# Kernel tuning notes

Measured on AMD Instinct MI355X. Metric: run time of the kernel, lower is better.

## Reference

```python
import jax, jax.numpy as jnp
import numpy as np

EPS = 1e-12  # F.normalize eps
WIN_SIZE = 200
WIN_STEP = 30  # eval mode (training uses 10)
N_WIN = 30     # 31 windows from length-1100 axis, last one dropped


def setup_inputs() -> dict:
    key = jax.random.key(0)
    ks = jax.random.split(key, 6)
    dim, K, out_dim = 128, 64, 256
    N, H, W = 8, 16, 900
    s = 1.0 / np.sqrt(dim)
    return {
        "x": jax.random.normal(ks[0], (N, dim, H, W), dtype=jnp.float32),
        "cluster_centers": jax.random.uniform(ks[1], (K, dim), dtype=jnp.float32),
        "conv_w": jax.random.normal(ks[2], (K, dim), dtype=jnp.float32) * s,
        "conv_b": jax.random.normal(ks[3], (K,), dtype=jnp.float32) * s,
        "mlp_w": jax.random.normal(ks[4], (out_dim, K * dim), dtype=jnp.float32) * s,
        "mlp_b": jax.random.normal(ks[5], (out_dim,), dtype=jnp.float32) * s,
    }


def _l2norm(v, axis):
    return v / jnp.clip(jnp.linalg.norm(v, axis=axis, keepdims=True), EPS)


def reference(x, cluster_centers, conv_w, conv_b, mlp_w, mlp_b):
    N, C, H, W = x.shape
    K = conv_w.shape[0]
    # 1x1 conv -> soft assignment, softmax over clusters (dim=1 after view(N,K,HW))
    logits = jnp.einsum('nchw,kc->nkhw', x, conv_w) + conv_b[None, :, None, None]
    a = jax.nn.softmax(logits, axis=1)  # (N,K,H,W)
    # Fused weighted residual sum over H (torch sums dim=-2 of (N,K,C,H,W)):
    # vlad_pre[n,k,c,w] = sum_h a[n,k,h,w]*x[n,c,h,w] - centers[k,c]*sum_h a[n,k,h,w]
    wx = jnp.einsum('nkhw,nchw->nkcw', a, x)               # (N,K,C,W)
    asum = a.sum(axis=2)                                    # (N,K,W)
    res = wx - cluster_centers[None, :, :, None] * asum[:, :, None, :]
    # circular pad along yaw: [800:] ++ all ++ [:100] -> length 1100
    res = jnp.concatenate([res[..., 800:], res, res[..., :100]], axis=-1)
    # sliding-window sum, size 200 step 30, drop last window -> 30 windows
    cs = jnp.cumsum(res, axis=-1)
    cs = jnp.concatenate([jnp.zeros(res.shape[:-1] + (1,), res.dtype), cs], axis=-1)
    starts = jnp.arange(N_WIN) * WIN_STEP
    win = cs[..., starts + WIN_SIZE] - cs[..., starts]      # (N,K,C,30)
    vlad = jnp.transpose(win, (0, 3, 1, 2)).reshape(N * N_WIN, K, C)
    vlad = _l2norm(vlad, axis=2)                            # intra-norm per cluster
    vlad = _l2norm(vlad.reshape(N * N_WIN, K * C), axis=1)  # global norm
    out = vlad @ mlp_w.T + mlp_b
    out = _l2norm(out, axis=1)
    return out.reshape(N, N_WIN, -1)
```

## Files before the change

kernel.cpp:

```cpp
#include <hip/hip_runtime.h>
#include <cstddef>

#define EPSF 1e-12f
#define NCB 90
#define NT 30
#define ODIM 256
#define DDIM 8192

typedef unsigned short u16;
typedef __attribute__((ext_vector_type(8))) short short8;
typedef __attribute__((ext_vector_type(4))) float float4v;

__device__ inline u16 f2bf(float f) {
  union { float f; unsigned u; } v; v.f = f;
  unsigned r = v.u + 0x7FFFu + ((v.u >> 16) & 1u);
  return (u16)(r >> 16);
}
__device__ inline float bf2f(u16 h) {
  union { unsigned u; float f; } v; v.u = ((unsigned)h) << 16;
  return v.f;
}

__global__ __launch_bounds__(512, 2) void k1_assign(
    const float* __restrict__ x,
    const float* __restrict__ conv_w,
    const float* __restrict__ conv_b,
    float* __restrict__ P,
    float* __restrict__ PA)
{
  __shared__ __align__(16) char smem[81408];

  const int bx0 = blockIdx.x;
  const int n = bx0 & 7;
  const int q = bx0 >> 3;
  const int t = threadIdx.x;
  const int lane = t & 63;
  const int w8 = t >> 6;

  const float* xn0 = x + (size_t)n * 1843200 + (size_t)(3 * q) * 10;

  const int colt = w8 & 1;
  const int kt = w8 >> 1;
  const int kr = kt * 16 + (lane & 15);
  const float bk = conv_b[kr];

  short8 wh[4], wl[4];
  {
    const int cbase = (lane >> 4) << 3;
#pragma unroll
    for (int cb32 = 0; cb32 < 4; ++cb32) {
      const float* wp = conv_w + (size_t)kr * 128 + cb32 * 32 + cbase;
      float4 u0 = *(const float4*)wp;
      float4 u1 = *(const float4*)(wp + 4);
      float fv[8] = {u0.x, u0.y, u0.z, u0.w, u1.x, u1.y, u1.z, u1.w};
      union { u16 u[8]; short8 v; } hh, ll;
#pragma unroll
      for (int j = 0; j < 8; ++j) {
        u16 h = f2bf(fv[j]);
        hh.u[j] = h;
        ll.u[j] = f2bf(fv[j] - bf2f(h));
      }
      wh[cb32] = hh.v; wl[cb32] = ll.v;
    }
  }

  float4v pacc[3][4];
#pragma unroll
  for (int si = 0; si < 3; ++si)
#pragma unroll
    for (int i = 0; i < 4; ++i) pacc[si][i] = (float4v){0.f, 0.f, 0.f, 0.f};
  float pak[3] = {0.f, 0.f, 0.f};

  float2 xr[3][4];
#pragma unroll
  for (int s = 0; s < 4; ++s) {
    int e2 = t + 512 * s;
    int c = e2 >> 4, p = e2 & 15;
    int cl = 2 * p;
    int h = cl / 10, wi = cl - 10 * h;
    const float* ap = xn0 + (size_t)c * 14400 + h * 900 + wi;
#pragma unroll
    for (int si = 0; si < 3; ++si)
      xr[si][s] = *(const float2*)(ap + si * 10);
  }

  for (int cc = 0; cc < 5; ++cc) {
    __syncthreads();
#pragma unroll
    for (int s = 0; s < 4; ++s) {
      int e2 = t + 512 * s;
      int c = e2 >> 4, p = e2 & 15;
      int cl = 2 * p;
      int ip = (c >> 4) * 640 + (p >> 2) * 160 + (c & 15) * 8 + (cl & 7);
      int F = (p >> 3) * 4 + (c >> 5);
      int L = (((c >> 3) & 3) << 4) + (cl & 15);
      int i0 = F * 520 + L * 8 + (c & 7);
#pragma unroll
      for (int si = 0; si < 3; ++si) {
        u16 h0 = f2bf(xr[si][s].x), h1 = f2bf(xr[si][s].y);
        u16* xf = (u16*)(smem + si * 27136 + 8320);
        u16* xtf = (u16*)(smem + si * 27136);
        ushort2 pr; pr.x = h0; pr.y = h1;
        *(ushort2*)&xf[ip] = pr;
        xtf[i0] = h0;
        xtf[i0 + 8] = h1;
      }
    }
    if (cc < 4) {
#pragma unroll
      for (int s = 0; s < 4; ++s) {
        int e2 = t + 512 * s;
        int c = e2 >> 4, p = e2 & 15;
        int g = (cc + 1) * 32 + 2 * p;
        int h = g / 10, wi = g - 10 * h;
        const float* ap = xn0 + (size_t)c * 14400 + h * 900 + wi;
#pragma unroll
        for (int si = 0; si < 3; ++si)
          xr[si][s] = *(const float2*)(ap + si * 10);
      }
    }
    __syncthreads();

    {
      float4v d0[3];
#pragma unroll
      for (int si = 0; si < 3; ++si) d0[si] = (float4v){0.f, 0.f, 0.f, 0.f};
#pragma unroll
      for (int cb32 = 0; cb32 < 4; ++cb32) {
#pragma unroll
        for (int si = 0; si < 3; ++si) {
          const u16* xtf = (const u16*)(smem + si * 27136);
          short8 xa = *(short8*)&xtf[(colt * 4 + cb32) * 520 + lane * 8];
          d0[si] = __builtin_amdgcn_mfma_f32_16x16x32_bf16(xa, wh[cb32], d0[si], 0, 0, 0);
          d0[si] = __builtin_amdgcn_mfma_f32_16x16x32_bf16(xa, wl[cb32], d0[si], 0, 0, 0);
        }
      }
      int colb = colt * 16 + ((lane >> 4) << 2);
#pragma unroll
      for (int si = 0; si < 3; ++si) {
        float* As = (float*)(smem + si * 27136 + 18560);
#pragma unroll
        for (int r = 0; r < 4; ++r)
          As[kr * 33 + colb + r] = d0[si][r] + bk;
      }
    }
    __syncthreads();

#pragma unroll
    for (int si = 0; si < 3; ++si) {
      float* As = (float*)(smem + si * 27136 + 18560);
      float* invs = (float*)(smem + si * 27136 + 27008);
      u16* afr = (u16*)(smem + si * 27136);
      {
        const int col4 = lane & 3;
        const int kq = lane >> 2;
        const int colg = w8 * 4 + col4;
        float m = -3.4e38f;
#pragma unroll
        for (int i = 0; i < 4; ++i) m = fmaxf(m, As[(kq * 4 + i) * 33 + colg]);
        m = fmaxf(m, __shfl_xor(m, 4));
        m = fmaxf(m, __shfl_xor(m, 8));
        m = fmaxf(m, __shfl_xor(m, 16));
        m = fmaxf(m, __shfl_xor(m, 32));
        float s = 0.f;
#pragma unroll
        for (int i = 0; i < 4; ++i) {
          int a = (kq * 4 + i) * 33 + colg;
          float e = __expf(As[a] - m);
          As[a] = e;
          s += e;
        }
        s += __shfl_xor(s, 4);
        s += __shfl_xor(s, 8);
        s += __shfl_xor(s, 16);
        s += __shfl_xor(s, 32);
        if (kq == 0) invs[colg] = 1.f / s;
      }
      {
        union { u16 u[4]; ushort4 v; } cvt;
        float paks = 0.f;
#pragma unroll
        for (int j = 0; j < 4; ++j) {
          float a = As[lane * 33 + w8 * 4 + j] * invs[w8 * 4 + j];
          paks += a;
          cvt.u[j] = f2bf(a);
        }
        pak[si] += paks;
        int dst = ((lane >> 4) * 64 + ((w8 >> 1) << 4) + (lane & 15)) * 8 + (w8 & 1) * 4;
        *(ushort4*)&afr[dst] = cvt.v;
      }
    }
    __syncthreads();

#pragma unroll
    for (int si = 0; si < 3; ++si) {
      const u16* afr = (const u16*)(smem + si * 27136);
      const u16* xf = (const u16*)(smem + si * 27136 + 8320);
      short8 aa = *(short8*)&afr[((w8 >> 1) * 64 + lane) * 8];
#pragma unroll
      for (int c4 = 0; c4 < 4; ++c4) {
        int ct = (w8 & 1) * 4 + c4;
        short8 xb = *(short8*)&xf[ct * 640 + (lane >> 4) * 160 + (lane & 15) * 8];
        pacc[si][c4] = __builtin_amdgcn_mfma_f32_16x16x32_bf16(aa, xb, pacc[si][c4], 0, 0, 0);
      }
    }
  }

  {
    int krow = (w8 >> 1) * 16 + ((lane >> 4) << 2);
    int c0 = (w8 & 1) * 64 + (lane & 15);
#pragma unroll
    for (int si = 0; si < 3; ++si) {
      float* Pp = P + (size_t)(n * NCB + 3 * q + si) * DDIM;
#pragma unroll
      for (int c4 = 0; c4 < 4; ++c4)
#pragma unroll
        for (int r = 0; r < 4; ++r)
          Pp[(krow + r) * 128 + c0 + c4 * 16] = pacc[si][c4][r];
    }
  }
  __syncthreads();
#pragma unroll
  for (int si = 0; si < 3; ++si)
    ((float*)(smem + si * 27136 + 18560))[t] = pak[si];
  __syncthreads();
  if (t < 64) {
#pragma unroll
    for (int si = 0; si < 3; ++si) {
      const float* pasum = (const float*)(smem + si * 27136 + 18560);
      float s = 0.f;
#pragma unroll
      for (int i = 0; i < 8; ++i) s += pasum[t + 64 * i];
      PA[(size_t)(n * NCB + 3 * q + si) * 64 + t] = s;
    }
  }
}

__global__ __launch_bounds__(256) void k2_vlad(
    const float* __restrict__ P, const float* __restrict__ PA,
    const float* __restrict__ centers, u16* __restrict__ vlad16,
    float* __restrict__ gss)
{
  __shared__ float Ak[8];
  __shared__ float red[4];
  const int bx0 = blockIdx.x;
  const int id = (bx0 & 7) * 240 + (bx0 >> 3);
  const int n = id / 240;
  const int rem = id - n * 240;
  const int wt = rem >> 3, eb = rem & 7;
  const int win = n * NT + wt;
  const int t = threadIdx.x;

  if (t < 32) {
    int kk = t >> 2, ii = t & 3;
    float s = 0.f;
#pragma unroll
    for (int ss = 0; ss < 5; ++ss) {
      int i = ii + 4 * ss;
      int cb = (3 * wt + 80 + i) % 90;
      s += PA[((size_t)n * NCB + cb) * 64 + eb * 8 + kk];
    }
    s += __shfl_xor(s, 1);
    s += __shfl_xor(s, 2);
    if (ii == 0) Ak[kk] = s;
  }
  __syncthreads();

  const int e0 = eb * 1024 + t * 4;
  const float* base = P + (size_t)n * NCB * DDIM + e0;
  float v[4];
#pragma unroll
  for (int j = 0; j < 4; ++j) v[j] = 0.f;
#pragma unroll 5
  for (int i = 0; i < 20; ++i) {
    int cb = (3 * wt + 80 + i) % 90;
    float4 u0 = *(const float4*)(base + (size_t)cb * DDIM);
    v[0] += u0.x; v[1] += u0.y; v[2] += u0.z; v[3] += u0.w;
  }

  const float A = Ak[t >> 5];
  const float* ce = centers + e0;
  float ss8 = 0.f;
#pragma unroll
  for (int j = 0; j < 4; ++j) {
    float val = v[j] - ce[j] * A;
    v[j] = val;
    ss8 += val * val;
  }
  float ssg = ss8;
  ssg += __shfl_xor(ssg, 1);
  ssg += __shfl_xor(ssg, 2);
  ssg += __shfl_xor(ssg, 4);
  ssg += __shfl_xor(ssg, 8);
  ssg += __shfl_xor(ssg, 16);
  float rn = 1.f / fmaxf(sqrtf(ssg), EPSF);
  float ts = ss8 * rn * rn;
  ts += __shfl_xor(ts, 1);
  ts += __shfl_xor(ts, 2);
  ts += __shfl_xor(ts, 4);
  ts += __shfl_xor(ts, 8);
  ts += __shfl_xor(ts, 16);
  ts += __shfl_xor(ts, 32);
  if ((t & 63) == 0) red[t >> 6] = ts;
  __syncthreads();
  if (t == 0) gss[(size_t)win * 8 + eb] = red[0] + red[1] + red[2] + red[3];

  union { u16 u[4]; ushort4 v4; } o;
#pragma unroll
  for (int j = 0; j < 4; ++j) o.u[j] = f2bf(v[j] * rn);
  *(ushort4*)(vlad16 + (size_t)win * DDIM + e0) = o.v4;
}

__global__ __launch_bounds__(256) void k3_gemm(
    const u16* __restrict__ vlad16, const float* __restrict__ gss,
    const float* __restrict__ mlp_w, float* __restrict__ part)
{
  __shared__ float ga[48];
  const int bx = blockIdx.x;
  const int xcd = bx & 7;
  const int q = bx >> 3;
  const int rtg = q % 5;
  const int h = (q / 5) * 8 + xcd;
  const int ot = h & 1;
  const int ks = h >> 1;
  const int t = threadIdx.x;
  const int lane = t & 63;
  const int w = t >> 6;

  if (t < 48) {
    int r = rtg * 48 + t;
    float s = 0.f;
#pragma unroll
    for (int j = 0; j < 8; ++j) s += gss[(size_t)r * 8 + j];
    ga[t] = 1.f / fmaxf(sqrtf(s), EPSF);
  }
  __syncthreads();

  const int m = lane & 15;
  const int kg = lane >> 4;
  const int d0 = ks * 256 + kg * 8;
  const u16* a0 = vlad16 + (size_t)(rtg * 48 + m) * DDIM + d0;

  float4v acc[3][2];
#pragma unroll
  for (int mi = 0; mi < 3; ++mi)
#pragma unroll
    for (int i = 0; i < 2; ++i) acc[mi][i] = (float4v){0.f, 0.f, 0.f, 0.f};

#pragma unroll
  for (int ko = 0; ko < 8; ++ko) {
    short8 a[3];
#pragma unroll
    for (int mi = 0; mi < 3; ++mi)
      a[mi] = *(const short8*)(a0 + (size_t)(mi * 16) * DDIM + ko * 32);
#pragma unroll
    for (int nt = 0; nt < 2; ++nt) {
      int o = ot * 128 + w * 32 + nt * 16 + m;
      const float* wrow = mlp_w + (size_t)o * DDIM + d0 + ko * 32;
      float4 u0 = *(const float4*)wrow;
      float4 u1 = *(const float4*)(wrow + 4);
      union { u16 u[8]; short8 v; } bb;
      bb.u[0] = f2bf(u0.x); bb.u[1] = f2bf(u0.y); bb.u[2] = f2bf(u0.z); bb.u[3] = f2bf(u0.w);
      bb.u[4] = f2bf(u1.x); bb.u[5] = f2bf(u1.y); bb.u[6] = f2bf(u1.z); bb.u[7] = f2bf(u1.w);
#pragma unroll
      for (int mi = 0; mi < 3; ++mi)
        acc[mi][nt] = __builtin_amdgcn_mfma_f32_16x16x32_bf16(a[mi], bb.v, acc[mi][nt], 0, 0, 0);
    }
  }

  float* pp = part + ((size_t)ks * 240 + rtg * 48) * ODIM;
#pragma unroll
  for (int mi = 0; mi < 3; ++mi)
#pragma unroll
    for (int nt = 0; nt < 2; ++nt) {
      int o = ot * 128 + w * 32 + nt * 16 + m;
#pragma unroll
      for (int r = 0; r < 4; ++r) {
        int rl = mi * 16 + kg * 4 + r;
        pp[rl * ODIM + o] = acc[mi][nt][r] * ga[rl];
      }
    }
}

__global__ __launch_bounds__(1024) void k4_out(
    const float* __restrict__ part, const float* __restrict__ bias,
    float* __restrict__ out)
{
  __shared__ float acc[4][256];
  __shared__ float red[4];
  const int r = blockIdx.x;
  const int t = threadIdx.x;
  const int o = t & 255, sq = t >> 8;

  float v = 0.f;
#pragma unroll
  for (int s = 0; s < 8; ++s)
    v += part[((size_t)(sq * 8 + s) * 240 + r) * ODIM + o];
  acc[sq][o] = v;
  __syncthreads();

  float ss = 0.f;
  if (t < 256) {
    v = acc[0][o] + acc[1][o] + acc[2][o] + acc[3][o] + bias[o];
    ss = v * v;
    ss += __shfl_xor(ss, 32);
    ss += __shfl_xor(ss, 16);
    ss += __shfl_xor(ss, 8);
    ss += __shfl_xor(ss, 4);
    ss += __shfl_xor(ss, 2);
    ss += __shfl_xor(ss, 1);
    if ((o & 63) == 0) red[t >> 6] = ss;
  }
  __syncthreads();
  if (t < 256) {
    float total = red[0] + red[1] + red[2] + red[3];
    out[(size_t)r * ODIM + o] = v / fmaxf(sqrtf(total), EPSF);
  }
}

extern "C" void kernel_launch(void* const* d_in, const int* in_sizes, int n_in,
                              void* d_out, int out_size, void* d_ws, size_t ws_size,
                              hipStream_t stream) {
  const float* x       = (const float*)d_in[0];
  const float* centers = (const float*)d_in[1];
  const float* conv_w  = (const float*)d_in[2];
  const float* conv_b  = (const float*)d_in[3];
  const float* mlp_w   = (const float*)d_in[4];
  const float* mlp_b   = (const float*)d_in[5];
  float* out = (float*)d_out;

  float* ws     = (float*)d_ws;
  float* P      = ws;
  float* PA     = ws + 5898240;
  u16*   vlad16 = (u16*)(ws + 5944320);
  float* gss    = (float*)(ws + 6927360);
  float* part   = ws;

  k1_assign<<<dim3(240),        dim3(512),  0, stream>>>(x, conv_w, conv_b, P, PA);
  k2_vlad  <<<dim3(8 * NT * 8), dim3(256),  0, stream>>>(P, PA, centers, vlad16, gss);
  k3_gemm  <<<dim3(320),        dim3(256),  0, stream>>>(vlad16, gss, mlp_w, part);
  k4_out   <<<dim3(240),        dim3(1024), 0, stream>>>(part, mlp_b, out);
}
```

Measured before the change: 154.7 us.

## Fuse four kernels into one cooperative kernel with grid-wide syncs

Merges the assignment, VLAD window/normalization, GEMM and output-normalization kernels into a single cooperative launch of 240 blocks of 512 threads, separated by grid.sync barriers. The later stages are remapped onto the 240 blocks (two 256-thread groups per block for VLAD and GEMM, 160 active blocks for GEMM). This removes three kernel-launch gaps and their tail effects. In exchange it adds grid-barrier cost and reduced parallelism in the later stages, and it relies on all 240 blocks being co-resident.

```diff
diff --git a/kernel.cpp b/kernel.cpp
--- a/kernel.cpp
+++ b/kernel.cpp
@@ -1,5 +1,8 @@
 #include <hip/hip_runtime.h>
+#include <hip/hip_cooperative_groups.h>
 #include <cstddef>
+
+namespace cg = cooperative_groups;
 
 #define EPSF 1e-12f
 #define NCB 90
@@ -21,400 +24,405 @@
   return v.f;
 }
 
-__global__ __launch_bounds__(512, 2) void k1_assign(
+__global__ __launch_bounds__(512, 2) void fused_all(
     const float* __restrict__ x,
     const float* __restrict__ conv_w,
     const float* __restrict__ conv_b,
+    const float* __restrict__ centers,
+    const float* __restrict__ mlp_w,
+    const float* __restrict__ mlp_b,
     float* __restrict__ P,
-    float* __restrict__ PA)
+    float* __restrict__ PA,
+    u16* __restrict__ vlad16,
+    float* __restrict__ gss,
+    float* __restrict__ part,
+    float* __restrict__ out)
 {
+  cg::grid_group grid = cg::this_grid();
   __shared__ __align__(16) char smem[81408];
-
   const int bx0 = blockIdx.x;
-  const int n = bx0 & 7;
-  const int q = bx0 >> 3;
   const int t = threadIdx.x;
   const int lane = t & 63;
   const int w8 = t >> 6;
 
-  const float* xn0 = x + (size_t)n * 1843200 + (size_t)(3 * q) * 10;
-
-  const int colt = w8 & 1;
-  const int kt = w8 >> 1;
-  const int kr = kt * 16 + (lane & 15);
-  const float bk = conv_b[kr];
-
-  short8 wh[4], wl[4];
   {
-    const int cbase = (lane >> 4) << 3;
-#pragma unroll
-    for (int cb32 = 0; cb32 < 4; ++cb32) {
-      const float* wp = conv_w + (size_t)kr * 128 + cb32 * 32 + cbase;
-      float4 u0 = *(const float4*)wp;
-      float4 u1 = *(const float4*)(wp + 4);
-      float fv[8] = {u0.x, u0.y, u0.z, u0.w, u1.x, u1.y, u1.z, u1.w};
-      union { u16 u[8]; short8 v; } hh, ll;
-#pragma unroll
-      for (int j = 0; j < 8; ++j) {
-        u16 h = f2bf(fv[j]);
-        hh.u[j] = h;
-        ll.u[j] = f2bf(fv[j] - bf2f(h));
-      }
-      wh[cb32] = hh.v; wl[cb32] = ll.v;
-    }
-  }
-
-  float4v pacc[3][4];
-#pragma unroll
-  for (int si = 0; si < 3; ++si)
-#pragma unroll
-    for (int i = 0; i < 4; ++i) pacc[si][i] = (float4v){0.f, 0.f, 0.f, 0.f};
-  float pak[3] = {0.f, 0.f, 0.f};
-
-  float2 xr[3][4];
-#pragma unroll
-  for (int s = 0; s < 4; ++s) {
-    int e2 = t + 512 * s;
-    int c = e2 >> 4, p = e2 & 15;
-    int cl = 2 * p;
-    int h = cl / 10, wi = cl - 10 * h;
-    const float* ap = xn0 + (size_t)c * 14400 + h * 900 + wi;
+    const int n = bx0 & 7;
+    const int q = bx0 >> 3;
+
+    const float* xn0 = x + (size_t)n * 1843200 + (size_t)(3 * q) * 10;
+
+    const int colt = w8 & 1;
+    const int kt = w8 >> 1;
+    const int kr = kt * 16 + (lane & 15);
+    const float bk = conv_b[kr];
+
+    short8 wh[4], wl[4];
+    {
+      const int cbase = (lane >> 4) << 3;
+#pragma unroll
+      for (int cb32 = 0; cb32 < 4; ++cb32) {
+        const float* wp = conv_w + (size_t)kr * 128 + cb32 * 32 + cbase;
+        float4 u0 = *(const float4*)wp;
+        float4 u1 = *(const float4*)(wp + 4);
+        float fv[8] = {u0.x, u0.y, u0.z, u0.w, u1.x, u1.y, u1.z, u1.w};
+        union { u16 u[8]; short8 v; } hh, ll;
+#pragma unroll
+        for (int j = 0; j < 8; ++j) {
+          u16 h = f2bf(fv[j]);
+          hh.u[j] = h;
+          ll.u[j] = f2bf(fv[j] - bf2f(h));
+        }
+        wh[cb32] = hh.v; wl[cb32] = ll.v;
+      }
+    }
+
+    float4v pacc[3][4];
 #pragma unroll
     for (int si = 0; si < 3; ++si)
-      xr[si][s] = *(const float2*)(ap + si * 10);
-  }
-
-  for (int cc = 0; cc < 5; ++cc) {
-    __syncthreads();
+#pragma unroll
+      for (int i = 0; i < 4; ++i) pacc[si][i] = (float4v){0.f, 0.f, 0.f, 0.f};
+    float pak[3] = {0.f, 0.f, 0.f};
+
+    float2 xr[3][4];
 #pragma unroll
     for (int s = 0; s < 4; ++s) {
       int e2 = t + 512 * s;
       int c = e2 >> 4, p = e2 & 15;
       int cl = 2 * p;
-      int ip = (c >> 4) * 640 + (p >> 2) * 160 + (c & 15) * 8 + (cl & 7);
-      int F = (p >> 3) * 4 + (c >> 5);
-      int L = (((c >> 3) & 3) << 4) + (cl & 15);
-      int i0 = F * 520 + L * 8 + (c & 7);
-#pragma unroll
-      for (int si = 0; si < 3; ++si) {
-        u16 h0 = f2bf(xr[si][s].x), h1 = f2bf(xr[si][s].y);
-        u16* xf = (u16*)(smem + si * 27136 + 8320);
-        u16* xtf = (u16*)(smem + si * 27136);
-        ushort2 pr; pr.x = h0; pr.y = h1;
-        *(ushort2*)&xf[ip] = pr;
-        xtf[i0] = h0;
-        xtf[i0 + 8] = h1;
-      }
-    }
-    if (cc < 4) {
+      int h = cl / 10, wi = cl - 10 * h;
+      const float* ap = xn0 + (size_t)c * 14400 + h * 900 + wi;
+#pragma unroll
+      for (int si = 0; si < 3; ++si)
+        xr[si][s] = *(const float2*)(ap + si * 10);
+    }
+
+    for (int cc = 0; cc < 5; ++cc) {
+      __syncthreads();
 #pragma unroll
       for (int s = 0; s < 4; ++s) {
         int e2 = t + 512 * s;
         int c = e2 >> 4, p = e2 & 15;
-        int g = (cc + 1) * 32 + 2 * p;
-        int h = g / 10, wi = g - 10 * h;
-        const float* ap = xn0 + (size_t)c * 14400 + h * 900 + wi;
-#pragma unroll
-        for (int si = 0; si < 3; ++si)
-          xr[si][s] = *(const float2*)(ap + si * 10);
-      }
-    }
-    __syncthreads();
-
-    {
-      float4v d0[3];
-#pragma unroll
-      for (int si = 0; si < 3; ++si) d0[si] = (float4v){0.f, 0.f, 0.f, 0.f};
-#pragma unroll
-      for (int cb32 = 0; cb32 < 4; ++cb32) {
+        int cl = 2 * p;
+        int ip = (c >> 4) * 640 + (p >> 2) * 160 + (c & 15) * 8 + (cl & 7);
+        int F = (p >> 3) * 4 + (c >> 5);
+        int L = (((c >> 3) & 3) << 4) + (cl & 15);
+        int i0 = F * 520 + L * 8 + (c & 7);
 #pragma unroll
         for (int si = 0; si < 3; ++si) {
-          const u16* xtf = (const u16*)(smem + si * 27136);
-          short8 xa = *(short8*)&xtf[(colt * 4 + cb32) * 520 + lane * 8];
-          d0[si] = __builtin_amdgcn_mfma_f32_16x16x32_bf16(xa, wh[cb32], d0[si], 0, 0, 0);
-          d0[si] = __builtin_amdgcn_mfma_f32_16x16x32_bf16(xa, wl[cb32], d0[si], 0, 0, 0);
-        }
-      }
-      int colb = colt * 16 + ((lane >> 4) << 2);
+          u16 h0 = f2bf(xr[si][s].x), h1 = f2bf(xr[si][s].y);
+          u16* xf = (u16*)(smem + si * 27136 + 8320);
+          u16* xtf = (u16*)(smem + si * 27136);
+          ushort2 pr; pr.x = h0; pr.y = h1;
+          *(ushort2*)&xf[ip] = pr;
+          xtf[i0] = h0;
+          xtf[i0 + 8] = h1;
+        }
+      }
+      if (cc < 4) {
+#pragma unroll
+        for (int s = 0; s < 4; ++s) {
+          int e2 = t + 512 * s;
+          int c = e2 >> 4, p = e2 & 15;
+          int g = (cc + 1) * 32 + 2 * p;
+          int h = g / 10, wi = g - 10 * h;
+          const float* ap = xn0 + (size_t)c * 14400 + h * 900 + wi;
+#pragma unroll
+          for (int si = 0; si < 3; ++si)
+            xr[si][s] = *(const float2*)(ap + si * 10);
+        }
+      }
+      __syncthreads();
+
+      {
+        float4v d0[3];
+#pragma unroll
+        for (int si = 0; si < 3; ++si) d0[si] = (float4v){0.f, 0.f, 0.f, 0.f};
+#pragma unroll
+        for (int cb32 = 0; cb32 < 4; ++cb32) {
+#pragma unroll
+          for (int si = 0; si < 3; ++si) {
+            const u16* xtf = (const u16*)(smem + si * 27136);
+            short8 xa = *(short8*)&xtf[(colt * 4 + cb32) * 520 + lane * 8];
+            d0[si] = __builtin_amdgcn_mfma_f32_16x16x32_bf16(xa, wh[cb32], d0[si], 0, 0, 0);
+            d0[si] = __builtin_amdgcn_mfma_f32_16x16x32_bf16(xa, wl[cb32], d0[si], 0, 0, 0);
+          }
+        }
+        int colb = colt * 16 + ((lane >> 4) << 2);
+#pragma unroll
+        for (int si = 0; si < 3; ++si) {
+          float* As = (float*)(smem + si * 27136 + 18560);
+#pragma unroll
+          for (int r = 0; r < 4; ++r)
+            As[kr * 33 + colb + r] = d0[si][r] + bk;
+        }
+      }
+      __syncthreads();
+
 #pragma unroll
       for (int si = 0; si < 3; ++si) {
         float* As = (float*)(smem + si * 27136 + 18560);
-#pragma unroll
-        for (int r = 0; r < 4; ++r)
-          As[kr * 33 + colb + r] = d0[si][r] + bk;
+        float* invs = (float*)(smem + si * 27136 + 27008);
+        u16* afr = (u16*)(smem + si * 27136);
+        {
+          const int col4 = lane & 3;
+          const int kq = lane >> 2;
+          const int colg = w8 * 4 + col4;
+          float m = -3.4e38f;
+#pragma unroll
+          for (int i = 0; i < 4; ++i) m = fmaxf(m, As[(kq * 4 + i) * 33 + colg]);
+          m = fmaxf(m, __shfl_xor(m, 4));
+          m = fmaxf(m, __shfl_xor(m, 8));
+          m = fmaxf(m, __shfl_xor(m, 16));
+          m = fmaxf(m, __shfl_xor(m, 32));
+          float s = 0.f;
+#pragma unroll
+          for (int i = 0; i < 4; ++i) {
+            int a = (kq * 4 + i) * 33 + colg;
+            float e = __expf(As[a] - m);
+            As[a] = e;
+            s += e;
+          }
+          s += __shfl_xor(s, 4);
+          s += __shfl_xor(s, 8);
+          s += __shfl_xor(s, 16);
+          s += __shfl_xor(s, 32);
+          if (kq == 0) invs[colg] = 1.f / s;
+        }
+        {
+          union { u16 u[4]; ushort4 v; } cvt;
+          float paks = 0.f;
+#pragma unroll
+          for (int j = 0; j < 4; ++j) {
+            float a = As[lane * 33 + w8 * 4 + j] * invs[w8 * 4 + j];
+            paks += a;
+            cvt.u[j] = f2bf(a);
+          }
+          pak[si] += paks;
+          int dst = ((lane >> 4) * 64 + ((w8 >> 1) << 4) + (lane & 15)) * 8 + (w8 & 1) * 4;
+          *(ushort4*)&afr[dst] = cvt.v;
+        }
+      }
+      __syncthreads();
+
+#pragma unroll
+      for (int si = 0; si < 3; ++si) {
+        const u16* afr = (const u16*)(smem + si * 27136);
+        const u16* xf = (const u16*)(smem + si * 27136 + 8320);
+        short8 aa = *(short8*)&afr[((w8 >> 1) * 64 + lane) * 8];
+#pragma unroll
+        for (int c4 = 0; c4 < 4; ++c4) {
+          int ct = (w8 & 1) * 4 + c4;
+          short8 xb = *(short8*)&xf[ct * 640 + (lane >> 4) * 160 + (lane & 15) * 8];
+          pacc[si][c4] = __builtin_amdgcn_mfma_f32_16x16x32_bf16(aa, xb, pacc[si][c4], 0, 0, 0);
+        }
+      }
+    }
+
+    {
+      int krow = (w8 >> 1) * 16 + ((lane >> 4) << 2);
+      int c0 = (w8 & 1) * 64 + (lane & 15);
+#pragma unroll
+      for (int si = 0; si < 3; ++si) {
+        float* Pp = P + (size_t)(n * NCB + 3 * q + si) * DDIM;
+#pragma unroll
+        for (int c4 = 0; c4 < 4; ++c4)
+#pragma unroll
+          for (int r = 0; r < 4; ++r)
+            Pp[(krow + r) * 128 + c0 + c4 * 16] = pacc[si][c4][r];
       }
     }
     __syncthreads();
-
-#pragma unroll
-    for (int si = 0; si < 3; ++si) {
-      float* As = (float*)(smem + si * 27136 + 18560);
-      float* invs = (float*)(smem + si * 27136 + 27008);
-      u16* afr = (u16*)(smem + si * 27136);
-      {
-        const int col4 = lane & 3;
-        const int kq = lane >> 2;
-        const int colg = w8 * 4 + col4;
-        float m = -3.4e38f;
-#pragma unroll
-        for (int i = 0; i < 4; ++i) m = fmaxf(m, As[(kq * 4 + i) * 33 + colg]);
-        m = fmaxf(m, __shfl_xor(m, 4));
-        m = fmaxf(m, __shfl_xor(m, 8));
-        m = fmaxf(m, __shfl_xor(m, 16));
-        m = fmaxf(m, __shfl_xor(m, 32));
+#pragma unroll
+    for (int si = 0; si < 3; ++si)
+      ((float*)(smem + si * 27136 + 18560))[t] = pak[si];
+    __syncthreads();
+    if (t < 64) {
+#pragma unroll
+      for (int si = 0; si < 3; ++si) {
+        const float* pasum = (const float*)(smem + si * 27136 + 18560);
         float s = 0.f;
 #pragma unroll
-        for (int i = 0; i < 4; ++i) {
-          int a = (kq * 4 + i) * 33 + colg;
-          float e = __expf(As[a] - m);
-          As[a] = e;
-          s += e;
-        }
-        s += __shfl_xor(s, 4);
-        s += __shfl_xor(s, 8);
-        s += __shfl_xor(s, 16);
-        s += __shfl_xor(s, 32);
-        if (kq == 0) invs[colg] = 1.f / s;
-      }
-      {
-        union { u16 u[4]; ushort4 v; } cvt;
-        float paks = 0.f;
-#pragma unroll
-        for (int j = 0; j < 4; ++j) {
-          float a = As[lane * 33 + w8 * 4 + j] * invs[w8 * 4 + j];
-          paks += a;
-          cvt.u[j] = f2bf(a);
-        }
-        pak[si] += paks;
-        int dst = ((lane >> 4) * 64 + ((w8 >> 1) << 4) + (lane & 15)) * 8 + (w8 & 1) * 4;
-        *(ushort4*)&afr[dst] = cvt.v;
-      }
+        for (int i = 0; i < 8; ++i) s += pasum[t + 64 * i];
+        PA[(size_t)(n * NCB + 3 * q + si) * 64 + t] = s;
+      }
+    }
+  }
+
+  grid.sync();
+
+  {
+    const int n = bx0 & 7, wt = bx0 >> 3;
+    const int g = t >> 8, t8 = t & 255;
+    const int win = n * NT + wt;
+    float* Ak = (float*)(smem + g * 32);
+    float* red = (float*)(smem + 64 + g * 16);
+
+    for (int i = 0; i < 4; ++i) {
+      const int eb = g + 2 * i;
+      __syncthreads();
+      if (t8 < 32) {
+        int kk = t8 >> 2, ii = t8 & 3;
+        float s = 0.f;
+#pragma unroll
+        for (int ss = 0; ss < 5; ++ss) {
+          int ix = ii + 4 * ss;
+          int cb = (3 * wt + 80 + ix) % 90;
+          s += PA[((size_t)n * NCB + cb) * 64 + eb * 8 + kk];
+        }
+        s += __shfl_xor(s, 1);
+        s += __shfl_xor(s, 2);
+        if (ii == 0) Ak[kk] = s;
+      }
+      __syncthreads();
+
+      const int e0 = eb * 1024 + t8 * 4;
+      const float* base = P + (size_t)n * NCB * DDIM + e0;
+      float v[4];
+#pragma unroll
+      for (int j = 0; j < 4; ++j) v[j] = 0.f;
+#pragma unroll 5
+      for (int i2 = 0; i2 < 20; ++i2) {
+        int cb = (3 * wt + 80 + i2) % 90;
+        float4 u0 = *(const float4*)(base + (size_t)cb * DDIM);
+        v[0] += u0.x; v[1] += u0.y; v[2] += u0.z; v[3] += u0.w;
+      }
+
+      const float A = Ak[t8 >> 5];
+      const float* ce = centers + e0;
+      float ss8 = 0.f;
+#pragma unroll
+      for (int j = 0; j < 4; ++j) {
+        float val = v[j] - ce[j] * A;
+        v[j] = val;
+        ss8 += val * val;
+      }
+      float ssg = ss8;
+      ssg += __shfl_xor(ssg, 1);
+      ssg += __shfl_xor(ssg, 2);
+      ssg += __shfl_xor(ssg, 4);
+      ssg += __shfl_xor(ssg, 8);
+      ssg += __shfl_xor(ssg, 16);
+      float rn = 1.f / fmaxf(sqrtf(ssg), EPSF);
+      float ts = ss8 * rn * rn;
+      ts += __shfl_xor(ts, 1);
+      ts += __shfl_xor(ts, 2);
+      ts += __shfl_xor(ts, 4);
+      ts += __shfl_xor(ts, 8);
+      ts += __shfl_xor(ts, 16);
+      ts += __shfl_xor(ts, 32);
+      if ((t8 & 63) == 0) red[t8 >> 6] = ts;
+      __syncthreads();
+      if (t8 == 0) gss[(size_t)win * 8 + eb] = red[0] + red[1] + red[2] + red[3];
+
+      union { u16 u[4]; ushort4 v4; } o;
+#pragma unroll
+      for (int j = 0; j < 4; ++j) o.u[j] = f2bf(v[j] * rn);
+      *(ushort4*)(vlad16 + (size_t)win * DDIM + e0) = o.v4;
+    }
+  }
+
+  grid.sync();
+
+  if (bx0 < 160) {
+    const int g = t >> 8, t8 = t & 255;
+    const int G = bx0 * 2 + g;
+    const int xcd = G & 7;
+    const int q3 = G >> 3;
+    const int rtg = q3 % 5;
+    const int h = (q3 / 5) * 8 + xcd;
+    const int ot = h & 1;
+    const int ks = h >> 1;
+    const int lane8 = t8 & 63;
+    const int w = t8 >> 6;
+    float* ga = (float*)(smem + 128 + g * 192);
+
+    if (t8 < 48) {
+      int r = rtg * 48 + t8;
+      float s = 0.f;
+#pragma unroll
+      for (int j = 0; j < 8; ++j) s += gss[(size_t)r * 8 + j];
+      ga[t8] = 1.f / fmaxf(sqrtf(s), EPSF);
     }
     __syncthreads();
 
-#pragma unroll
-    for (int si = 0; si < 3; ++si) {
-      const u16* afr = (const u16*)(smem + si * 27136);
-      const u16* xf = (const u16*)(smem + si * 27136 + 8320);
-      short8 aa = *(short8*)&afr[((w8 >> 1) * 64 + lane) * 8];
-#pragma unroll
-      for (int c4 = 0; c4 < 4; ++c4) {
-        int ct = (w8 & 1) * 4 + c4;
-        short8 xb = *(short8*)&xf[ct * 640 + (lane >> 4) * 160 + (lane & 15) * 8];
-        pacc[si][c4] = __builtin_amdgcn_mfma_f32_16x16x32_bf16(aa, xb, pacc[si][c4], 0, 0, 0);
-      }
-    }
+    const int m = lane8 & 15;
+    const int kg = lane8 >> 4;
+    const int d0 = ks * 256 + kg * 8;
+    const u16* a0 = vlad16 + (size_t)(rtg * 48 + m) * DDIM + d0;
+
+    float4v acc[3][2];
+#pragma unroll
+    for (int mi = 0; mi < 3; ++mi)
+#pragma unroll
+      for (int i = 0; i < 2; ++i) acc[mi][i] = (float4v){0.f, 0.f, 0.f, 0.f};
+
+#pragma unroll
+    for (int ko = 0; ko < 8; ++ko) {
+      short8 a[3];
+#pragma unroll
+      for (int mi = 0; mi < 3; ++mi)
+        a[mi] = *(const short8*)(a0 + (size_t)(mi * 16) * DDIM + ko * 32);
+#pragma unroll
+      for (int nt = 0; nt < 2; ++nt) {
+        int o = ot * 128 + w * 32 + nt * 16 + m;
+        const float* wrow = mlp_w + (size_t)o * DDIM + d0 + ko * 32;
+        float4 u0 = *(const float4*)wrow;
+        float4 u1 = *(const float4*)(wrow + 4);
+        union { u16 u[8]; short8 v; } bb;
+        bb.u[0] = f2bf(u0.x); bb.u[1] = f2bf(u0.y); bb.u[2] = f2bf(u0.z); bb.u[3] = f2bf(u0.w);
+        bb.u[4] = f2bf(u1.x); bb.u[5] = f2bf(u1.y); bb.u[6] = f2bf(u1.z); bb.u[7] = f2bf(u1.w);
+#pragma unroll
+        for (int mi = 0; mi < 3; ++mi)
+          acc[mi][nt] = __builtin_amdgcn_mfma_f32_16x16x32_bf16(a[mi], bb.v, acc[mi][nt], 0, 0, 0);
+      }
+    }
+
+    float* pp = part + ((size_t)ks * 240 + rtg * 48) * ODIM;
+#pragma unroll
+    for (int mi = 0; mi < 3; ++mi)
+#pragma unroll
+      for (int nt = 0; nt < 2; ++nt) {
+        int o = ot * 128 + w * 32 + nt * 16 + m;
+#pragma unroll
+        for (int r = 0; r < 4; ++r) {
+          int rl = mi * 16 + kg * 4 + r;
+          pp[rl * ODIM + o] = acc[mi][nt][r] * ga[rl];
+        }
+      }
   }
 
+  grid.sync();
+
   {
-    int krow = (w8 >> 1) * 16 + ((lane >> 4) << 2);
-    int c0 = (w8 & 1) * 64 + (lane & 15);
-#pragma unroll
-    for (int si = 0; si < 3; ++si) {
-      float* Pp = P + (size_t)(n * NCB + 3 * q + si) * DDIM;
-#pragma unroll
-      for (int c4 = 0; c4 < 4; ++c4)
-#pragma unroll
-        for (int r = 0; r < 4; ++r)
-          Pp[(krow + r) * 128 + c0 + c4 * 16] = pacc[si][c4][r];
-    }
-  }
-  __syncthreads();
-#pragma unroll
-  for (int si = 0; si < 3; ++si)
-    ((float*)(smem + si * 27136 + 18560))[t] = pak[si];
-  __syncthreads();
-  if (t < 64) {
-#pragma unroll
-    for (int si = 0; si < 3; ++si) {
-      const float* pasum = (const float*)(smem + si * 27136 + 18560);
-      float s = 0.f;
-#pragma unroll
-      for (int i = 0; i < 8; ++i) s += pasum[t + 64 * i];
-      PA[(size_t)(n * NCB + 3 * q + si) * 64 + t] = s;
-    }
-  }
-}
-
-__global__ __launch_bounds__(256) void k2_vlad(
-    const float* __restrict__ P, const float* __restrict__ PA,
-    const float* __restrict__ centers, u16* __restrict__ vlad16,
-    float* __restrict__ gss)
-{
-  __shared__ float Ak[8];
-  __shared__ float red[4];
-  const int bx0 = blockIdx.x;
-  const int id = (bx0 & 7) * 240 + (bx0 >> 3);
-  const int n = id / 240;
-  const int rem = id - n * 240;
-  const int wt = rem >> 3, eb = rem & 7;
-  const int win = n * NT + wt;
-  const int t = threadIdx.x;
-
-  if (t < 32) {
-    int kk = t >> 2, ii = t & 3;
-    float s = 0.f;
-#pragma unroll
-    for (int ss = 0; ss < 5; ++ss) {
-      int i = ii + 4 * ss;
-      int cb = (3 * wt + 80 + i) % 90;
-      s += PA[((size_t)n * NCB + cb) * 64 + eb * 8 + kk];
-    }
-    s += __shfl_xor(s, 1);
-    s += __shfl_xor(s, 2);
-    if (ii == 0) Ak[kk] = s;
-  }
-  __syncthreads();
-
-  const int e0 = eb * 1024 + t * 4;
-  const float* base = P + (size_t)n * NCB * DDIM + e0;
-  float v[4];
-#pragma unroll
-  for (int j = 0; j < 4; ++j) v[j] = 0.f;
-#pragma unroll 5
-  for (int i = 0; i < 20; ++i) {
-    int cb = (3 * wt + 80 + i) % 90;
-    float4 u0 = *(const float4*)(base + (size_t)cb * DDIM);
-    v[0] += u0.x; v[1] += u0.y; v[2] += u0.z; v[3] += u0.w;
-  }
-
-  const float A = Ak[t >> 5];
-  const float* ce = centers + e0;
-  float ss8 = 0.f;
-#pragma unroll
-  for (int j = 0; j < 4; ++j) {
-    float val = v[j] - ce[j] * A;
-    v[j] = val;
-    ss8 += val * val;
-  }
-  float ssg = ss8;
-  ssg += __shfl_xor(ssg, 1);
-  ssg += __shfl_xor(ssg, 2);
-  ssg += __shfl_xor(ssg, 4);
-  ssg += __shfl_xor(ssg, 8);
-  ssg += __shfl_xor(ssg, 16);
-  float rn = 1.f / fmaxf(sqrtf(ssg), EPSF);
-  float ts = ss8 * rn * rn;
-  ts += __shfl_xor(ts, 1);
-  ts += __shfl_xor(ts, 2);
-  ts += __shfl_xor(ts, 4);
-  ts += __shfl_xor(ts, 8);
-  ts += __shfl_xor(ts, 16);
-  ts += __shfl_xor(ts, 32);
-  if ((t & 63) == 0) red[t >> 6] = ts;
-  __syncthreads();
-  if (t == 0) gss[(size_t)win * 8 + eb] = red[0] + red[1] + red[2] + red[3];
-
-  union { u16 u[4]; ushort4 v4; } o;
-#pragma unroll
-  for (int j = 0; j < 4; ++j) o.u[j] = f2bf(v[j] * rn);
-  *(ushort4*)(vlad16 + (size_t)win * DDIM + e0) = o.v4;
-}
-
-__global__ __launch_bounds__(256) void k3_gemm(
-    const u16* __restrict__ vlad16, const float* __restrict__ gss,
-    const float* __restrict__ mlp_w, float* __restrict__ part)
-{
-  __shared__ float ga[48];
-  const int bx = blockIdx.x;
-  const int xcd = bx & 7;
-  const int q = bx >> 3;
-  const int rtg = q % 5;
-  const int h = (q / 5) * 8 + xcd;
-  const int ot = h & 1;
-  const int ks = h >> 1;
-  const int t = threadIdx.x;
-  const int lane = t & 63;
-  const int w = t >> 6;
-
-  if (t < 48) {
-    int r = rtg * 48 + t;
-    float s = 0.f;
-#pragma unroll
-    for (int j = 0; j < 8; ++j) s += gss[(size_t)r * 8 + j];
-    ga[t] = 1.f / fmaxf(sqrtf(s), EPSF);
-  }
-  __syncthreads();
-
-  const int m = lane & 15;
-  const int kg = lane >> 4;
-  const int d0 = ks * 256 + kg * 8;
-  const u16* a0 = vlad16 + (size_t)(rtg * 48 + m) * DDIM + d0;
-
-  float4v acc[3][2];
-#pragma unroll
-  for (int mi = 0; mi < 3; ++mi)
-#pragma unroll
-    for (int i = 0; i < 2; ++i) acc[mi][i] = (float4v){0.f, 0.f, 0.f, 0.f};
-
-#pragma unroll
-  for (int ko = 0; ko < 8; ++ko) {
-    short8 a[3];
-#pragma unroll
-    for (int mi = 0; mi < 3; ++mi)
-      a[mi] = *(const short8*)(a0 + (size_t)(mi * 16) * DDIM + ko * 32);
-#pragma unroll
-    for (int nt = 0; nt < 2; ++nt) {
-      int o = ot * 128 + w * 32 + nt * 16 + m;
-      const float* wrow = mlp_w + (size_t)o * DDIM + d0 + ko * 32;
-      float4 u0 = *(const float4*)wrow;
-      float4 u1 = *(const float4*)(wrow + 4);
-      union { u16 u[8]; short8 v; } bb;
-      bb.u[0] = f2bf(u0.x); bb.u[1] = f2bf(u0.y); bb.u[2] = f2bf(u0.z); bb.u[3] = f2bf(u0.w);
-      bb.u[4] = f2bf(u1.x); bb.u[5] = f2bf(u1.y); bb.u[6] = f2bf(u1.z); bb.u[7] = f2bf(u1.w);
-#pragma unroll
-      for (int mi = 0; mi < 3; ++mi)
-        acc[mi][nt] = __builtin_amdgcn_mfma_f32_16x16x32_bf16(a[mi], bb.v, acc[mi][nt], 0, 0, 0);
-    }
-  }
-
-  float* pp = part + ((size_t)ks * 240 + rtg * 48) * ODIM;
-#pragma unroll
-  for (int mi = 0; mi < 3; ++mi)
-#pragma unroll
-    for (int nt = 0; nt < 2; ++nt) {
-      int o = ot * 128 + w * 32 + nt * 16 + m;
-#pragma unroll
-      for (int r = 0; r < 4; ++r) {
-        int rl = mi * 16 + kg * 4 + r;
-        pp[rl * ODIM + o] = acc[mi][nt][r] * ga[rl];
-      }
-    }
-}
-
-__global__ __launch_bounds__(1024) void k4_out(
-    const float* __restrict__ part, const float* __restrict__ bias,
-    float* __restrict__ out)
-{
-  __shared__ float acc[4][256];
-  __shared__ float red[4];
-  const int r = blockIdx.x;
-  const int t = threadIdx.x;
-  const int o = t & 255, sq = t >> 8;
-
-  float v = 0.f;
-#pragma unroll
-  for (int s = 0; s < 8; ++s)
-    v += part[((size_t)(sq * 8 + s) * 240 + r) * ODIM + o];
-  acc[sq][o] = v;
-  __syncthreads();
-
-  float ss = 0.f;
-  if (t < 256) {
-    v = acc[0][o] + acc[1][o] + acc[2][o] + acc[3][o] + bias[o];
-    ss = v * v;
-    ss += __shfl_xor(ss, 32);
-    ss += __shfl_xor(ss, 16);
-    ss += __shfl_xor(ss, 8);
-    ss += __shfl_xor(ss, 4);
-    ss += __shfl_xor(ss, 2);
-    ss += __shfl_xor(ss, 1);
-    if ((o & 63) == 0) red[t >> 6] = ss;
-  }
-  __syncthreads();
-  if (t < 256) {
-    float total = red[0] + red[1] + red[2] + red[3];
-    out[(size_t)r * ODIM + o] = v / fmaxf(sqrtf(total), EPSF);
+    const int r = bx0;
+    const int o = t & 255, sq = t >> 8;
+    float* acc = (float*)smem;
+    float* red2 = (float*)(smem + 2048);
+
+    float v = 0.f;
+#pragma unroll
+    for (int s = 0; s < 16; ++s)
+      v += part[((size_t)(sq * 16 + s) * 240 + r) * ODIM + o];
+    acc[sq * 256 + o] = v;
+    __syncthreads();
+
+    float vv = 0.f;
+    if (t < 256) {
+      vv = acc[o] + acc[256 + o] + mlp_b[o];
+      float ss = vv * vv;
+      ss += __shfl_xor(ss, 32);
+      ss += __shfl_xor(ss, 16);
+      ss += __shfl_xor(ss, 8);
+      ss += __shfl_xor(ss, 4);
+      ss += __shfl_xor(ss, 2);
+      ss += __shfl_xor(ss, 1);
+      if ((t & 63) == 0) red2[t >> 6] = ss;
+    }
+    __syncthreads();
+    if (t < 256) {
+      float total = red2[0] + red2[1] + red2[2] + red2[3];
+      out[(size_t)r * ODIM + o] = vv / fmaxf(sqrtf(total), EPSF);
+    }
   }
 }
 
@@ -436,8 +444,11 @@
   float* gss    = (float*)(ws + 6927360);
   float* part   = ws;
 
-  k1_assign<<<dim3(240),        dim3(512),  0, stream>>>(x, conv_w, conv_b, P, PA);
-  k2_vlad  <<<dim3(8 * NT * 8), dim3(256),  0, stream>>>(P, PA, centers, vlad16, gss);
-  k3_gemm  <<<dim3(320),        dim3(256),  0, stream>>>(vlad16, gss, mlp_w, part);
-  k4_out   <<<dim3(240),        dim3(1024), 0, stream>>>(part, mlp_b, out);
+  void* kargs[] = {
+    (void*)&x, (void*)&conv_w, (void*)&conv_b, (void*)&centers,
+    (void*)&mlp_w, (void*)&mlp_b, (void*)&P, (void*)&PA,
+    (void*)&vlad16, (void*)&gss, (void*)&part, (void*)&out
+  };
+  hipLaunchCooperativeKernel((void*)fused_all, dim3(240), dim3(512),
+                             kargs, 0, stream);
 }
```

Measured after the change: 262.2 us. +69.4%, slower.
